# Kernel optimization log

Hardware: AMD Instinct MI355X
Metric: run time of the kernel (lower is better)

## Reference

```python
import jax, jax.numpy as jnp
import numpy as np


def setup_inputs() -> dict:
    key = jax.random.key(0)
    k1, k2, k3 = jax.random.split(key, 3)
    bs, seqlen, hidden = 2, 2048, 1024
    s, h = 4, 256  # sqrt_n_heads, head_size
    std = 0.02
    num_layers = 12
    hidden_states = jax.random.normal(k1, (bs, seqlen, hidden), dtype=jnp.float32)
    q_scale = 1.0 / np.sqrt(2.0 * num_layers * h)
    queries = jax.random.normal(k2, (s, h, h * s), dtype=jnp.float32) * std * q_scale
    combiners = jax.random.normal(k3, (s, h * s, h), dtype=jnp.float32) * (std * q_scale)
    return {"hidden_states": hidden_states, "queries": queries, "combiners": combiners}


def reference(hidden_states, queries, combiners):
    # queries: [s1, h, s*h], combiners: [s1, s*h, h]
    s, h, _ = queries.shape
    bs, S, E = hidden_states.shape
    x = hidden_states.reshape(bs, S, s, h)            # [b, t, s, h]
    qw = queries.reshape(s, h, s, h)                  # [s1, h_in, s2, h_out]
    # projected queries, already permuted to [s2, b, t, s1, f]
    Q = jnp.einsum('btae,aeqf->qbtaf', x, qw)
    # pre-attention scores: [s2, b, t, s1, u] (u = key position)  ~O(S^2)
    pre = jnp.einsum('qbtaf,buqf->qbtau', Q, x)
    # attention output, permuted to [s1, b, t, s2, g]
    attn = jnp.einsum('qbtau,buqg->abtqg', pre, x)
    attn = attn.reshape(s, bs, S, s * h)              # [s1, b, t, s2*h]
    out = jnp.einsum('abtk,akg->btag', attn, combiners)
    return out.reshape(bs, S, s * h)
```

## Files before the change

kernel.cpp:

```cpp
#include <hip/hip_runtime.h>
#include <hip/hip_bf16.h>


typedef unsigned short u16;
using short8  = __attribute__((ext_vector_type(8))) short;
using floatx4 = __attribute__((ext_vector_type(4))) float;

__device__ inline u16 f2bf(float f) {
    unsigned u = __float_as_uint(f);
    unsigned r = u + 0x7fffu + ((u >> 16) & 1u);
    return (u16)(r >> 16);
}

__device__ inline void stage64_bf(const u16* __restrict__ src, long ld,
                                  u16* __restrict__ dst, int tid) {
#pragma unroll
    for (int it = 0; it < 2; ++it) {
        const int flat = (it * 256 + tid) * 8;
        const int kl = flat & 63, rl = flat >> 6;
        const short8 v = *(const short8*)&src[(long)rl * ld + kl];
        const int chunk = ((kl >> 5) * 4 + (rl >> 4)) * 64 + ((kl >> 3) & 3) * 16 + (rl & 15);
        *(short8*)&dst[chunk * 8] = v;
    }
}

template <typename TC, int KR>
__device__ inline void gemm64(const u16* __restrict__ A, long lda,
                              const u16* __restrict__ B, long ldb,
                              TC* __restrict__ C, long ldc,
                              int m0, int n0) {
    __shared__ u16 As[16384];
    __shared__ u16 Bs[16384];
    const int tid = threadIdx.x, lane = tid & 63, w = tid >> 6;
    const int IA = (w & 1) * 2, JB = (w >> 1) * 2;
    floatx4 acc[2][2] = {};

#pragma unroll
    for (int r = 0; r < KR; ++r) {
        if (r) __syncthreads();
        const u16* Ar = A + r * 256;
        const u16* Br = B + r * 256;
#pragma unroll
        for (int kb = 0; kb < 4; ++kb) {
            stage64_bf(Ar + kb * 64, lda, As + kb * 4096, tid);
            stage64_bf(Br + kb * 64, ldb, Bs + kb * 4096, tid);
        }
        __syncthreads();

#pragma unroll
        for (int kb = 0; kb < 4; ++kb)
#pragma unroll
            for (int s = 0; s < 2; ++s) {
                short8 af[2], bfr[2];
#pragma unroll
                for (int i = 0; i < 2; ++i)
                    af[i] = *(const short8*)&As[kb * 4096 + ((s * 4 + IA + i) * 64 + lane) * 8];
#pragma unroll
                for (int j = 0; j < 2; ++j)
                    bfr[j] = *(const short8*)&Bs[kb * 4096 + ((s * 4 + JB + j) * 64 + lane) * 8];
#pragma unroll
                for (int i = 0; i < 2; ++i)
#pragma unroll
                    for (int j = 0; j < 2; ++j)
                        acc[i][j] = __builtin_amdgcn_mfma_f32_16x16x32_bf16(af[i], bfr[j], acc[i][j], 0, 0, 0);
            }
    }

    const int rb = (lane >> 4) * 4, col = lane & 15;
#pragma unroll
    for (int i = 0; i < 2; ++i)
#pragma unroll
        for (int j = 0; j < 2; ++j)
#pragma unroll
            for (int r = 0; r < 4; ++r) {
                const int gm = m0 + (IA + i) * 16 + rb + r;
                const int gn = n0 + (JB + j) * 16 + col;
                TC* p = &C[(long)gm * ldc + gn];
                if (sizeof(TC) == 2) *(u16*)p = f2bf(acc[i][j][r]);
                else                 *(float*)p = acc[i][j][r];
            }
}

__global__ __launch_bounds__(256) void k_prep(const float* __restrict__ x,
                                              const float* __restrict__ qw,
                                              const float* __restrict__ comb,
                                              u16* __restrict__ xbf,
                                              u16* __restrict__ qwbf,
                                              u16* __restrict__ combt) {
    const int bx = blockIdx.x, tid = threadIdx.x;
    __shared__ u16 T[64][66];
    if (bx < 2560) {
        const float* src = bx < 2048 ? x : qw;
        u16* dst = bx < 2048 ? xbf : qwbf;
        const long i = ((long)(bx < 2048 ? bx : bx - 2048) * 256 + tid) * 8;
        const float4 a = *(const float4*)&src[i];
        const float4 b = *(const float4*)&src[i + 4];
        ushort4 lo, hi;
        lo.x = f2bf(a.x); lo.y = f2bf(a.y); lo.z = f2bf(a.z); lo.w = f2bf(a.w);
        hi.x = f2bf(b.x); hi.y = f2bf(b.y); hi.z = f2bf(b.z); hi.w = f2bf(b.w);
        *(ushort4*)&dst[i]     = lo;
        *(ushort4*)&dst[i + 4] = hi;
    } else {
        const int t = bx - 2560;
        const int a = t >> 6;
        const int qh0 = ((t >> 2) & 15) * 64, g0 = (t & 3) * 64;
        const float* src = comb + (long)a * 262144;
        u16* dst = combt + (long)a * 262144;
#pragma unroll
        for (int it = 0; it < 4; ++it) {
            const int flat = (it * 256 + tid) * 4;
            const int r = flat >> 6, c = flat & 63;
            const float4 f = *(const float4*)&src[(long)(qh0 + r) * 256 + g0 + c];
            T[r][c]     = f2bf(f.x); T[r][c + 1] = f2bf(f.y);
            T[r][c + 2] = f2bf(f.z); T[r][c + 3] = f2bf(f.w);
        }
        __syncthreads();
#pragma unroll
        for (int it = 0; it < 4; ++it) {
            const int flat = (it * 256 + tid) * 4;
            const int r = flat >> 6, c = flat & 63;
            ushort4 v;
            v.x = T[c][r]; v.y = T[c + 1][r]; v.z = T[c + 2][r]; v.w = T[c + 3][r];
            *(ushort4*)&dst[(long)(g0 + r) * 1024 + qh0 + c] = v;
        }
    }
}

__global__ __launch_bounds__(256) void k_gred(const float* __restrict__ Gp,
                                              u16* __restrict__ Gs) {
    const long i = ((long)blockIdx.x * 256 + threadIdx.x) * 4;
    float4 acc = *(const float4*)&Gp[i];
#pragma unroll
    for (int s = 1; s < 8; ++s) {
        const float4 f = *(const float4*)&Gp[(long)s * 524288 + i];
        acc.x += f.x; acc.y += f.y; acc.z += f.z; acc.w += f.w;
    }
    ushort4 v;
    v.x = f2bf(acc.x); v.y = f2bf(acc.y); v.z = f2bf(acc.z); v.w = f2bf(acc.w);
    *(ushort4*)&Gs[i] = v;
}

__device__ inline void stage_km128_bf(const u16* __restrict__ src, long ld,
                                      u16* __restrict__ dst, int tid) {
#pragma unroll
    for (int it = 0; it < 4; ++it) {
        const int flat = (it * 256 + tid) * 8;
        const int m = flat & 127, k = flat >> 7;
        const short8 v = *(const short8*)&src[(long)k * ld + m];
        const int cb_ = ((k >> 5) * 8 + (m >> 4)) * 64 + ((k & 31) >> 3) * 16 + (m & 15);
        const int j = k & 7;
#pragma unroll
        for (int e = 0; e < 8; ++e)
            dst[(cb_ + e) * 8 + j] = (u16)v[e];
    }
}

__global__ __launch_bounds__(256) void k_gram(const u16* __restrict__ xbf,
                                              float* __restrict__ Gp) {
    __shared__ u16 As[16384];
    __shared__ u16 Bs[16384];
    const int tl = blockIdx.x, bq = blockIdx.y, split = blockIdx.z;
    const int tm = tl >> 1, tn = tl & 1;
    const int b = bq >> 2, q = bq & 3;
    const int tid = threadIdx.x, lane = tid & 63, w = tid >> 6;
    const int IA2 = (w & 1), JB2 = (w >> 1);

    const u16* base = xbf + (long)b * 2097152 + (long)split * 256 * 1024 + q * 256;
    const u16* A = base + tm * 128;
    const u16* B = base + tn * 128;
    floatx4 acc[4][4] = {};

#pragma unroll
    for (int burst = 0; burst < 2; ++burst) {
        if (burst) __syncthreads();
#pragma unroll
        for (int kb = 0; kb < 2; ++kb) {
            const long kk = burst * 128 + kb * 64;
            stage_km128_bf(A + kk * 1024, 1024, As + kb * 8192, tid);
            stage_km128_bf(B + kk * 1024, 1024, Bs + kb * 8192, tid);
        }
        __syncthreads();
#pragma unroll
        for (int kb = 0; kb < 2; ++kb)
#pragma unroll
            for (int s = 0; s < 2; ++s) {
                short8 af[4], bfr[4];
#pragma unroll
                for (int i = 0; i < 4; ++i)
                    af[i] = *(const short8*)&As[kb * 8192 + ((s * 8 + IA2 * 4 + i) * 64 + lane) * 8];
#pragma unroll
                for (int j = 0; j < 4; ++j)
                    bfr[j] = *(const short8*)&Bs[kb * 8192 + ((s * 8 + JB2 * 4 + j) * 64 + lane) * 8];
#pragma unroll
                for (int i = 0; i < 4; ++i)
#pragma unroll
                    for (int j = 0; j < 4; ++j)
                        acc[i][j] = __builtin_amdgcn_mfma_f32_16x16x32_bf16(af[i], bfr[j], acc[i][j], 0, 0, 0);
            }
    }

    float* C = Gp + (long)(split * 8 + bq) * 65536;
    const int rb = (lane >> 4) * 4, col = lane & 15;
#pragma unroll
    for (int i = 0; i < 4; ++i)
#pragma unroll
        for (int j = 0; j < 4; ++j)
#pragma unroll
            for (int r = 0; r < 4; ++r) {
                const int gm = tm * 128 + IA2 * 64 + i * 16 + rb + r;
                const int gn = tn * 128 + JB2 * 64 + j * 16 + col;
                C[(long)gm * 256 + gn] = acc[i][j][r];
            }
}

__global__ __launch_bounds__(256) void k_2a(const u16* __restrict__ combt,
                                            const u16* __restrict__ Gs,
                                            u16* __restrict__ Tt) {
    const int tile = blockIdx.x, i = blockIdx.y;
    const int tm = tile >> 2, tn = tile & 3;
    const int q = i & 3, ba = i >> 2, b = ba >> 2, a = ba & 3;
    gemm64<u16, 1>(
        combt + (long)a * 262144 + (long)tm * 64 * 1024 + q * 256, 1024,
        Gs + (long)(b * 4 + q) * 65536 + (long)tn * 64 * 256, 256,
        Tt + (long)ba * 262144, 1024,
        tm * 64, q * 256 + tn * 64);
}

__global__ __launch_bounds__(256) void k_2b(const u16* __restrict__ Tt,
                                            const u16* __restrict__ qwbf,
                                            u16* __restrict__ Wt) {
    const int tile = blockIdx.x, ba = blockIdx.y;
    const int tm = tile >> 2, tn = tile & 3;
    const int a = ba & 3;
    gemm64<u16, 4>(
        Tt + (long)ba * 262144 + (long)tm * 64 * 1024, 1024,
        qwbf + (long)a * 262144 + (long)tn * 64 * 1024, 1024,
        Wt + (long)ba * 65536, 256,
        tm * 64, tn * 64);
}

__global__ __launch_bounds__(256) void k_3(const u16* __restrict__ xbf,
                                           const u16* __restrict__ Wt,
                                           float* __restrict__ out) {
    const int tl = blockIdx.x, ba = blockIdx.y;
    const int tm = tl >> 2, tn = tl & 3;
    const int b = ba >> 2, a = ba & 3;
    gemm64<float, 1>(
        xbf + (long)b * 2097152 + (long)tm * 64 * 1024 + a * 256, 1024,
        Wt + (long)ba * 65536 + (long)tn * 64 * 256, 256,
        out + (long)b * 2097152 + a * 256, 1024,
        tm * 64, tn * 64);
}

extern "C" void kernel_launch(void* const* d_in, const int* in_sizes, int n_in,
                              void* d_out, int out_size, void* d_ws, size_t ws_size,
                              hipStream_t stream) {
    const float* x    = (const float*)d_in[0];
    const float* qw   = (const float*)d_in[1];
    const float* comb = (const float*)d_in[2];
    float* out = (float*)d_out;

    char* ws = (char*)d_ws;
    float* Gp   = (float*)(ws);
    u16*   xbf  = (u16*)  (ws + (16u << 20));
    u16*   Tt   = (u16*)  (ws + (24u << 20));
    u16*   qwbf = (u16*)  (ws + (28u << 20));
    u16*   combt= (u16*)  (ws + (30u << 20));
    u16*   Gsbf = (u16*)  (ws + (32u << 20));
    u16*   Wtbf = (u16*)  (ws + (33u << 20));

    k_prep<<<dim3(2816),    256, 0, stream>>>(x, qw, comb, xbf, qwbf, combt);
    k_gram<<<dim3(4, 8, 8), 256, 0, stream>>>(xbf, Gp);
    k_gred<<<dim3(512),     256, 0, stream>>>(Gp, Gsbf);
    k_2a  <<<dim3(16, 32),  256, 0, stream>>>(combt, Gsbf, Tt);
    k_2b  <<<dim3(16, 8),   256, 0, stream>>>(Tt, qwbf, Wtbf);
    k_3   <<<dim3(128, 8),  256, 0, stream>>>(xbf, Wtbf, out);
}
```

Before: 132.1 us.

## Fuse six kernel launches into one persistent kernel with grid-wide barriers

Merges the prep, Gram, reduction, two weight-GEMM and output-GEMM kernels into a single persistent kernel of 512 blocks. Stages are separated by an atomic-counter grid barrier, and the counter is reset with a memset before each launch. The goal is to remove the launch gaps and tail effects between the six small kernels. The cost is that many blocks sit idle in stages that use few of them, and correctness depends on all 512 blocks being co-resident (launch bounds set to 2 blocks per CU).

```diff
diff --git a/kernel.cpp b/kernel.cpp
--- a/kernel.cpp
+++ b/kernel.cpp
@@ -1,15 +1,29 @@
 #include <hip/hip_runtime.h>
-#include <hip/hip_bf16.h>
 
 
 typedef unsigned short u16;
 using short8  = __attribute__((ext_vector_type(8))) short;
 using floatx4 = __attribute__((ext_vector_type(4))) float;
+
+#define NB 512
 
 __device__ inline u16 f2bf(float f) {
     unsigned u = __float_as_uint(f);
     unsigned r = u + 0x7fffu + ((u >> 16) & 1u);
     return (u16)(r >> 16);
+}
+
+__device__ inline void gbar(unsigned* __restrict__ cnt, unsigned target) {
+    __syncthreads();
+    if (threadIdx.x == 0) {
+        __threadfence();
+        atomicAdd(cnt, 1u);
+        while (__hip_atomic_load(cnt, __ATOMIC_ACQUIRE,
+                                 __HIP_MEMORY_SCOPE_AGENT) < target)
+            __builtin_amdgcn_s_sleep(2);
+        __threadfence();
+    }
+    __syncthreads();
 }
 
 __device__ inline void stage64_bf(const u16* __restrict__ src, long ld,
@@ -24,20 +38,34 @@
     }
 }
 
+__device__ inline void stage_km128_bf(const u16* __restrict__ src, long ld,
+                                      u16* __restrict__ dst, int tid) {
+#pragma unroll
+    for (int it = 0; it < 4; ++it) {
+        const int flat = (it * 256 + tid) * 8;
+        const int m = flat & 127, k = flat >> 7;
+        const short8 v = *(const short8*)&src[(long)k * ld + m];
+        const int cb_ = ((k >> 5) * 8 + (m >> 4)) * 64 + ((k & 31) >> 3) * 16 + (m & 15);
+        const int j = k & 7;
+#pragma unroll
+        for (int e = 0; e < 8; ++e)
+            dst[(cb_ + e) * 8 + j] = (u16)v[e];
+    }
+}
+
 template <typename TC, int KR>
-__device__ inline void gemm64(const u16* __restrict__ A, long lda,
+__device__ inline void gemm64(u16* __restrict__ As, u16* __restrict__ Bs,
+                              const u16* __restrict__ A, long lda,
                               const u16* __restrict__ B, long ldb,
                               TC* __restrict__ C, long ldc,
                               int m0, int n0) {
-    __shared__ u16 As[16384];
-    __shared__ u16 Bs[16384];
     const int tid = threadIdx.x, lane = tid & 63, w = tid >> 6;
     const int IA = (w & 1) * 2, JB = (w >> 1) * 2;
     floatx4 acc[2][2] = {};
 
 #pragma unroll
     for (int r = 0; r < KR; ++r) {
-        if (r) __syncthreads();
+        __syncthreads();
         const u16* Ar = A + r * 256;
         const u16* Br = B + r * 256;
 #pragma unroll
@@ -81,175 +109,161 @@
             }
 }
 
-__global__ __launch_bounds__(256) void k_prep(const float* __restrict__ x,
-                                              const float* __restrict__ qw,
-                                              const float* __restrict__ comb,
-                                              u16* __restrict__ xbf,
-                                              u16* __restrict__ qwbf,
-                                              u16* __restrict__ combt) {
-    const int bx = blockIdx.x, tid = threadIdx.x;
-    __shared__ u16 T[64][66];
-    if (bx < 2560) {
-        const float* src = bx < 2048 ? x : qw;
-        u16* dst = bx < 2048 ? xbf : qwbf;
-        const long i = ((long)(bx < 2048 ? bx : bx - 2048) * 256 + tid) * 8;
-        const float4 a = *(const float4*)&src[i];
-        const float4 b = *(const float4*)&src[i + 4];
-        ushort4 lo, hi;
-        lo.x = f2bf(a.x); lo.y = f2bf(a.y); lo.z = f2bf(a.z); lo.w = f2bf(a.w);
-        hi.x = f2bf(b.x); hi.y = f2bf(b.y); hi.z = f2bf(b.z); hi.w = f2bf(b.w);
-        *(ushort4*)&dst[i]     = lo;
-        *(ushort4*)&dst[i + 4] = hi;
-    } else {
-        const int t = bx - 2560;
-        const int a = t >> 6;
-        const int qh0 = ((t >> 2) & 15) * 64, g0 = (t & 3) * 64;
-        const float* src = comb + (long)a * 262144;
-        u16* dst = combt + (long)a * 262144;
-#pragma unroll
-        for (int it = 0; it < 4; ++it) {
-            const int flat = (it * 256 + tid) * 4;
-            const int r = flat >> 6, c = flat & 63;
-            const float4 f = *(const float4*)&src[(long)(qh0 + r) * 256 + g0 + c];
-            T[r][c]     = f2bf(f.x); T[r][c + 1] = f2bf(f.y);
-            T[r][c + 2] = f2bf(f.z); T[r][c + 3] = f2bf(f.w);
-        }
-        __syncthreads();
-#pragma unroll
-        for (int it = 0; it < 4; ++it) {
-            const int flat = (it * 256 + tid) * 4;
-            const int r = flat >> 6, c = flat & 63;
-            ushort4 v;
-            v.x = T[c][r]; v.y = T[c + 1][r]; v.z = T[c + 2][r]; v.w = T[c + 3][r];
-            *(ushort4*)&dst[(long)(g0 + r) * 1024 + qh0 + c] = v;
-        }
-    }
-}
-
-__global__ __launch_bounds__(256) void k_gred(const float* __restrict__ Gp,
-                                              u16* __restrict__ Gs) {
-    const long i = ((long)blockIdx.x * 256 + threadIdx.x) * 4;
-    float4 acc = *(const float4*)&Gp[i];
-#pragma unroll
-    for (int s = 1; s < 8; ++s) {
-        const float4 f = *(const float4*)&Gp[(long)s * 524288 + i];
-        acc.x += f.x; acc.y += f.y; acc.z += f.z; acc.w += f.w;
-    }
-    ushort4 v;
-    v.x = f2bf(acc.x); v.y = f2bf(acc.y); v.z = f2bf(acc.z); v.w = f2bf(acc.w);
-    *(ushort4*)&Gs[i] = v;
-}
-
-__device__ inline void stage_km128_bf(const u16* __restrict__ src, long ld,
-                                      u16* __restrict__ dst, int tid) {
-#pragma unroll
-    for (int it = 0; it < 4; ++it) {
-        const int flat = (it * 256 + tid) * 8;
-        const int m = flat & 127, k = flat >> 7;
-        const short8 v = *(const short8*)&src[(long)k * ld + m];
-        const int cb_ = ((k >> 5) * 8 + (m >> 4)) * 64 + ((k & 31) >> 3) * 16 + (m & 15);
-        const int j = k & 7;
-#pragma unroll
-        for (int e = 0; e < 8; ++e)
-            dst[(cb_ + e) * 8 + j] = (u16)v[e];
-    }
-}
-
-__global__ __launch_bounds__(256) void k_gram(const u16* __restrict__ xbf,
-                                              float* __restrict__ Gp) {
+__global__ __launch_bounds__(256, 2) void k_all(
+        const float* __restrict__ x, const float* __restrict__ qw,
+        const float* __restrict__ comb, float* __restrict__ out,
+        float* __restrict__ Gp, u16* __restrict__ xbf, u16* __restrict__ Tt,
+        u16* __restrict__ qwbf, u16* __restrict__ combt,
+        u16* __restrict__ Gsbf, u16* __restrict__ Wtbf,
+        unsigned* __restrict__ bar) {
     __shared__ u16 As[16384];
     __shared__ u16 Bs[16384];
-    const int tl = blockIdx.x, bq = blockIdx.y, split = blockIdx.z;
-    const int tm = tl >> 1, tn = tl & 1;
-    const int b = bq >> 2, q = bq & 3;
-    const int tid = threadIdx.x, lane = tid & 63, w = tid >> 6;
-    const int IA2 = (w & 1), JB2 = (w >> 1);
-
-    const u16* base = xbf + (long)b * 2097152 + (long)split * 256 * 1024 + q * 256;
-    const u16* A = base + tm * 128;
-    const u16* B = base + tn * 128;
-    floatx4 acc[4][4] = {};
-
-#pragma unroll
-    for (int burst = 0; burst < 2; ++burst) {
-        if (burst) __syncthreads();
-#pragma unroll
-        for (int kb = 0; kb < 2; ++kb) {
-            const long kk = burst * 128 + kb * 64;
-            stage_km128_bf(A + kk * 1024, 1024, As + kb * 8192, tid);
-            stage_km128_bf(B + kk * 1024, 1024, Bs + kb * 8192, tid);
-        }
-        __syncthreads();
-#pragma unroll
-        for (int kb = 0; kb < 2; ++kb)
-#pragma unroll
-            for (int s = 0; s < 2; ++s) {
-                short8 af[4], bfr[4];
-#pragma unroll
-                for (int i = 0; i < 4; ++i)
-                    af[i] = *(const short8*)&As[kb * 8192 + ((s * 8 + IA2 * 4 + i) * 64 + lane) * 8];
-#pragma unroll
-                for (int j = 0; j < 4; ++j)
-                    bfr[j] = *(const short8*)&Bs[kb * 8192 + ((s * 8 + JB2 * 4 + j) * 64 + lane) * 8];
-#pragma unroll
-                for (int i = 0; i < 4; ++i)
+    const int bid = blockIdx.x, tid = threadIdx.x;
+
+    for (int u = bid; u < 2816; u += NB) {
+        if (u < 2560) {
+            const float* src = u < 2048 ? x : qw;
+            u16* dst = u < 2048 ? xbf : qwbf;
+            const long i = ((long)(u < 2048 ? u : u - 2048) * 256 + tid) * 8;
+            const float4 a = *(const float4*)&src[i];
+            const float4 b = *(const float4*)&src[i + 4];
+            ushort4 lo, hi;
+            lo.x = f2bf(a.x); lo.y = f2bf(a.y); lo.z = f2bf(a.z); lo.w = f2bf(a.w);
+            hi.x = f2bf(b.x); hi.y = f2bf(b.y); hi.z = f2bf(b.z); hi.w = f2bf(b.w);
+            *(ushort4*)&dst[i]     = lo;
+            *(ushort4*)&dst[i + 4] = hi;
+        } else {
+            u16 (*T)[66] = (u16(*)[66])As;
+            const int t = u - 2560;
+            const int a = t >> 6;
+            const int qh0 = ((t >> 2) & 15) * 64, g0 = (t & 3) * 64;
+            const float* src = comb + (long)a * 262144;
+            u16* dst = combt + (long)a * 262144;
+#pragma unroll
+            for (int it = 0; it < 4; ++it) {
+                const int flat = (it * 256 + tid) * 4;
+                const int r = flat >> 6, c = flat & 63;
+                const float4 f = *(const float4*)&src[(long)(qh0 + r) * 256 + g0 + c];
+                T[r][c]     = f2bf(f.x); T[r][c + 1] = f2bf(f.y);
+                T[r][c + 2] = f2bf(f.z); T[r][c + 3] = f2bf(f.w);
+            }
+            __syncthreads();
+#pragma unroll
+            for (int it = 0; it < 4; ++it) {
+                const int flat = (it * 256 + tid) * 4;
+                const int r = flat >> 6, c = flat & 63;
+                ushort4 v;
+                v.x = T[c][r]; v.y = T[c + 1][r]; v.z = T[c + 2][r]; v.w = T[c + 3][r];
+                *(ushort4*)&dst[(long)(g0 + r) * 1024 + qh0 + c] = v;
+            }
+        }
+    }
+    gbar(bar, 1 * NB);
+
+    if (bid < 256) {
+        const int tl = bid & 3, bq = (bid >> 2) & 7, split = bid >> 5;
+        const int tm = tl >> 1, tn = tl & 1;
+        const int b = bq >> 2, q = bq & 3;
+        const int lane = tid & 63, w = tid >> 6;
+        const int IA2 = (w & 1), JB2 = (w >> 1);
+
+        const u16* base = xbf + (long)b * 2097152 + (long)split * 256 * 1024 + q * 256;
+        const u16* A = base + tm * 128;
+        const u16* B = base + tn * 128;
+        floatx4 acc[4][4] = {};
+
+#pragma unroll
+        for (int burst = 0; burst < 2; ++burst) {
+            if (burst) __syncthreads();
+#pragma unroll
+            for (int kb = 0; kb < 2; ++kb) {
+                const long kk = burst * 128 + kb * 64;
+                stage_km128_bf(A + kk * 1024, 1024, As + kb * 8192, tid);
+                stage_km128_bf(B + kk * 1024, 1024, Bs + kb * 8192, tid);
+            }
+            __syncthreads();
+#pragma unroll
+            for (int kb = 0; kb < 2; ++kb)
+#pragma unroll
+                for (int s = 0; s < 2; ++s) {
+                    short8 af[4], bfr[4];
+#pragma unroll
+                    for (int i = 0; i < 4; ++i)
+                        af[i] = *(const short8*)&As[kb * 8192 + ((s * 8 + IA2 * 4 + i) * 64 + lane) * 8];
 #pragma unroll
                     for (int j = 0; j < 4; ++j)
-                        acc[i][j] = __builtin_amdgcn_mfma_f32_16x16x32_bf16(af[i], bfr[j], acc[i][j], 0, 0, 0);
-            }
-    }
-
-    float* C = Gp + (long)(split * 8 + bq) * 65536;
-    const int rb = (lane >> 4) * 4, col = lane & 15;
-#pragma unroll
-    for (int i = 0; i < 4; ++i)
-#pragma unroll
-        for (int j = 0; j < 4; ++j)
-#pragma unroll
-            for (int r = 0; r < 4; ++r) {
-                const int gm = tm * 128 + IA2 * 64 + i * 16 + rb + r;
-                const int gn = tn * 128 + JB2 * 64 + j * 16 + col;
-                C[(long)gm * 256 + gn] = acc[i][j][r];
-            }
-}
-
-__global__ __launch_bounds__(256) void k_2a(const u16* __restrict__ combt,
-                                            const u16* __restrict__ Gs,
-                                            u16* __restrict__ Tt) {
-    const int tile = blockIdx.x, i = blockIdx.y;
-    const int tm = tile >> 2, tn = tile & 3;
-    const int q = i & 3, ba = i >> 2, b = ba >> 2, a = ba & 3;
-    gemm64<u16, 1>(
-        combt + (long)a * 262144 + (long)tm * 64 * 1024 + q * 256, 1024,
-        Gs + (long)(b * 4 + q) * 65536 + (long)tn * 64 * 256, 256,
-        Tt + (long)ba * 262144, 1024,
-        tm * 64, q * 256 + tn * 64);
-}
-
-__global__ __launch_bounds__(256) void k_2b(const u16* __restrict__ Tt,
-                                            const u16* __restrict__ qwbf,
-                                            u16* __restrict__ Wt) {
-    const int tile = blockIdx.x, ba = blockIdx.y;
-    const int tm = tile >> 2, tn = tile & 3;
-    const int a = ba & 3;
-    gemm64<u16, 4>(
-        Tt + (long)ba * 262144 + (long)tm * 64 * 1024, 1024,
-        qwbf + (long)a * 262144 + (long)tn * 64 * 1024, 1024,
-        Wt + (long)ba * 65536, 256,
-        tm * 64, tn * 64);
-}
-
-__global__ __launch_bounds__(256) void k_3(const u16* __restrict__ xbf,
-                                           const u16* __restrict__ Wt,
-                                           float* __restrict__ out) {
-    const int tl = blockIdx.x, ba = blockIdx.y;
-    const int tm = tl >> 2, tn = tl & 3;
-    const int b = ba >> 2, a = ba & 3;
-    gemm64<float, 1>(
-        xbf + (long)b * 2097152 + (long)tm * 64 * 1024 + a * 256, 1024,
-        Wt + (long)ba * 65536 + (long)tn * 64 * 256, 256,
-        out + (long)b * 2097152 + a * 256, 1024,
-        tm * 64, tn * 64);
+                        bfr[j] = *(const short8*)&Bs[kb * 8192 + ((s * 8 + JB2 * 4 + j) * 64 + lane) * 8];
+#pragma unroll
+                    for (int i = 0; i < 4; ++i)
+#pragma unroll
+                        for (int j = 0; j < 4; ++j)
+                            acc[i][j] = __builtin_amdgcn_mfma_f32_16x16x32_bf16(af[i], bfr[j], acc[i][j], 0, 0, 0);
+                }
+        }
+
+        float* C = Gp + (long)(split * 8 + bq) * 65536;
+        const int rb = (lane >> 4) * 4, col = lane & 15;
+#pragma unroll
+        for (int i = 0; i < 4; ++i)
+#pragma unroll
+            for (int j = 0; j < 4; ++j)
+#pragma unroll
+                for (int r = 0; r < 4; ++r) {
+                    const int gm = tm * 128 + IA2 * 64 + i * 16 + rb + r;
+                    const int gn = tn * 128 + JB2 * 64 + j * 16 + col;
+                    C[(long)gm * 256 + gn] = acc[i][j][r];
+                }
+    }
+    gbar(bar, 2 * NB);
+
+    {
+        const long i = ((long)bid * 256 + tid) * 4;
+        float4 acc = *(const float4*)&Gp[i];
+#pragma unroll
+        for (int s = 1; s < 8; ++s) {
+            const float4 f = *(const float4*)&Gp[(long)s * 524288 + i];
+            acc.x += f.x; acc.y += f.y; acc.z += f.z; acc.w += f.w;
+        }
+        ushort4 v;
+        v.x = f2bf(acc.x); v.y = f2bf(acc.y); v.z = f2bf(acc.z); v.w = f2bf(acc.w);
+        *(ushort4*)&Gsbf[i] = v;
+    }
+    gbar(bar, 3 * NB);
+
+    {
+        const int tile = bid & 15, i = bid >> 4;
+        const int tm = tile >> 2, tn = tile & 3;
+        const int q = i & 3, ba = i >> 2, b = ba >> 2, a = ba & 3;
+        gemm64<u16, 1>(As, Bs,
+            combt + (long)a * 262144 + (long)tm * 64 * 1024 + q * 256, 1024,
+            Gsbf + (long)(b * 4 + q) * 65536 + (long)tn * 64 * 256, 256,
+            Tt + (long)ba * 262144, 1024,
+            tm * 64, q * 256 + tn * 64);
+    }
+    gbar(bar, 4 * NB);
+
+    if (bid < 128) {
+        const int tile = bid & 15, ba = bid >> 4;
+        const int tm = tile >> 2, tn = tile & 3;
+        const int a = ba & 3;
+        gemm64<u16, 4>(As, Bs,
+            Tt + (long)ba * 262144 + (long)tm * 64 * 1024, 1024,
+            qwbf + (long)a * 262144 + (long)tn * 64 * 1024, 1024,
+            Wtbf + (long)ba * 65536, 256,
+            tm * 64, tn * 64);
+    }
+    gbar(bar, 5 * NB);
+
+    for (int u = bid; u < 1024; u += NB) {
+        const int tl = u & 127, ba = u >> 7;
+        const int tm = tl >> 2, tn = tl & 3;
+        const int b = ba >> 2, a = ba & 3;
+        gemm64<float, 1>(As, Bs,
+            xbf + (long)b * 2097152 + (long)tm * 64 * 1024 + a * 256, 1024,
+            Wtbf + (long)ba * 65536 + (long)tn * 64 * 256, 256,
+            out + (long)b * 2097152 + a * 256, 1024,
+            tm * 64, tn * 64);
+    }
 }
 
 extern "C" void kernel_launch(void* const* d_in, const int* in_sizes, int n_in,
@@ -268,11 +282,10 @@
     u16*   combt= (u16*)  (ws + (30u << 20));
     u16*   Gsbf = (u16*)  (ws + (32u << 20));
     u16*   Wtbf = (u16*)  (ws + (33u << 20));
-
-    k_prep<<<dim3(2816),    256, 0, stream>>>(x, qw, comb, xbf, qwbf, combt);
-    k_gram<<<dim3(4, 8, 8), 256, 0, stream>>>(xbf, Gp);
-    k_gred<<<dim3(512),     256, 0, stream>>>(Gp, Gsbf);
-    k_2a  <<<dim3(16, 32),  256, 0, stream>>>(combt, Gsbf, Tt);
-    k_2b  <<<dim3(16, 8),   256, 0, stream>>>(Tt, qwbf, Wtbf);
-    k_3   <<<dim3(128, 8),  256, 0, stream>>>(xbf, Wtbf, out);
-}
+    unsigned* bar = (unsigned*)(ws + (34u << 20));
+
+    hipMemsetAsync(bar, 0, 256, stream);
+    k_all<<<dim3(NB), dim3(256), 0, stream>>>(x, qw, comb, out,
+                                              Gp, xbf, Tt, qwbf, combt,
+                                              Gsbf, Wtbf, bar);
+}
```

New measurement: 480.6 us. 264% more time.
